# Optimization experiments

Measured on AMD Instinct MI355X. Metric: run time of the kernel, lower is better.

## Reference

```python
import jax, jax.numpy as jnp
import numpy as np

N = 50000
E = 800000
IN_DIM = 128
HID = 128
HEADS = 8
OUT_DIM = 64
LRELU_SLOPE = 0.2


def setup_inputs() -> dict:
    key = jax.random.key(0)
    ks = jax.random.split(key, 10)
    x = jax.random.normal(ks[0], (N, IN_DIM), dtype=jnp.float32)
    edge_index = jax.random.randint(ks[1], (2, E), 0, N, dtype=jnp.int64)
    c1 = HID // HEADS  # 16
    W1 = jax.random.normal(ks[2], (IN_DIM, HID), dtype=jnp.float32) * (1.0 / np.sqrt(IN_DIM))
    as1 = jax.random.normal(ks[3], (HEADS, c1), dtype=jnp.float32) * 0.1
    ad1 = jax.random.normal(ks[4], (HEADS, c1), dtype=jnp.float32) * 0.1
    b1 = jnp.zeros((HID,), dtype=jnp.float32)
    W2 = jax.random.normal(ks[5], (HID, OUT_DIM), dtype=jnp.float32) * (1.0 / np.sqrt(HID))
    as2 = jax.random.normal(ks[6], (1, OUT_DIM), dtype=jnp.float32) * 0.1
    ad2 = jax.random.normal(ks[7], (1, OUT_DIM), dtype=jnp.float32) * 0.1
    b2 = jnp.zeros((OUT_DIM,), dtype=jnp.float32)
    return {"x": x, "edge_index": edge_index, "W1": W1, "as1": as1, "ad1": ad1,
            "b1": b1, "W2": W2, "as2": as2, "ad2": ad2, "b2": b2}


def gat_conv(x, src, dst, W, a_src, a_dst, b, heads, ch, concat):
    n = x.shape[0]
    h = (x @ W).reshape(n, heads, ch)               # [N,H,C]
    alpha_s = jnp.sum(h * a_src, axis=-1)           # [N,H]
    alpha_d = jnp.sum(h * a_dst, axis=-1)           # [N,H]
    e = jax.nn.leaky_relu(alpha_s[src] + alpha_d[dst], LRELU_SLOPE)  # [E,H]
    m = jax.ops.segment_max(e, dst, num_segments=n)  # per-dst max (self-loops guarantee nonempty)
    e = jnp.exp(e - m[dst])
    denom = jax.ops.segment_sum(e, dst, num_segments=n)
    alpha = e / (denom[dst] + 1e-16)                # [E,H]
    msg = h[src] * alpha[:, :, None]                # [E,H,C]
    out = jax.ops.segment_sum(msg, dst, num_segments=n)  # [N,H,C]
    out = out.reshape(n, heads * ch) if concat else out.mean(axis=1)
    return out + b


def reference(x, edge_index, W1, as1, ad1, b1, W2, as2, ad2, b2):
    n = x.shape[0]
    loops = jnp.arange(n, dtype=edge_index.dtype)
    src = jnp.concatenate([edge_index[0], loops])   # PyG GATConv adds self-loops
    dst = jnp.concatenate([edge_index[1], loops])
    # layer 1: GATBlock (dropout is identity at eval), heads=8, concat, ELU
    h = gat_conv(x, src, dst, W1, as1, ad1, b1, HEADS, HID // HEADS, True)
    h = jax.nn.elu(h)
    # final conv: heads=1, concat=False
    out = gat_conv(h, src, dst, W2, as2, ad2, b2, 1, OUT_DIM, False)
    return jax.nn.log_softmax(out, axis=1)
```

## Files before the change

kernel.cpp:

```cpp
#include <hip/hip_runtime.h>
#include <hip/hip_bf16.h>
#include <math.h>

#define IN_DIM 128
#define HID 128
#define HEADS 8
#define OUT_DIM 64
#define SLOPE 0.2f
#define BSHIFT 7
#define BCAP 4096
#define BCAPSHIFT 12
#define EPT 8
#define G1 256
#define G2 256

typedef short bf16x8 __attribute__((ext_vector_type(8)));
typedef float f32x4 __attribute__((ext_vector_type(4)));

__device__ __forceinline__ float lrelu(float x) { return fmaxf(x, SLOPE * x); }
__device__ __forceinline__ float bf2f(unsigned u) { return __uint_as_float(u << 16); }
__device__ __forceinline__ unsigned short f2bf(float f) {
    unsigned u = __float_as_uint(f);
    return (unsigned short)((u + 0x7FFF + ((u >> 16) & 1)) >> 16);
}

__device__ __forceinline__ void bscatter_body(
    int blk, int* smem, const int* __restrict__ idx,
    int* __restrict__ gcursor, unsigned* __restrict__ bucket_buf,
    int E, int N, int NB) {
    int* hist = smem;
    int* base = smem + 512;
    int* s_nz = smem + 1024;
    int t = threadIdx.x;
    for (int i = t; i < NB; i += 256) hist[i] = 0;
    if (t == 0) *s_nz = 0;
    __syncthreads();
    {
        int nz = (idx[2 * t + 1] != 0) + (idx[2 * t + 513] != 0);
        if (nz) atomicAdd(s_nz, nz);
    }
    __syncthreads();
    int flag = (*s_nz > 16) ? 1 : 0;
    int e0 = blk * (256 * EPT);
    int EN = E + N;
    unsigned ent[EPT];
    int bid[EPT];
    int loc[EPT];
#pragma unroll
    for (int k = 0; k < EPT; k++) {
        int e = e0 + k * 256 + t;
        bid[k] = -1;
        if (e < EN) {
            int src, dst;
            if (e < E) {
                if (flag) { src = idx[e]; dst = idx[E + e]; }
                else      { src = idx[2 * e]; dst = idx[2 * (E + e)]; }
            } else {
                src = dst = e - E;
            }
            int b = dst >> BSHIFT;
            bid[k] = b;
            ent[k] = ((unsigned)(dst & ((1 << BSHIFT) - 1)) << 16) | (unsigned)src;
            loc[k] = atomicAdd(&hist[b], 1);
        }
    }
    __syncthreads();
    for (int i = t; i < NB; i += 256) {
        int c = hist[i];
        if (c) base[i] = atomicAdd(&gcursor[i], c);
    }
    __syncthreads();
#pragma unroll
    for (int k = 0; k < EPT; k++) {
        if (bid[k] >= 0) {
            int pos = base[bid[k]] + loc[k];
            if (pos < BCAP) bucket_buf[((size_t)bid[k] << BCAPSHIFT) + pos] = ent[k];
        }
    }
}

__device__ __forceinline__ void gemm1_body(
    int blk, short* Wt, const float* __restrict__ x, const float* __restrict__ W1,
    unsigned short* __restrict__ h1g, int N) {
    int t = threadIdx.x;
    for (int id = t; id < 128 * 32; id += 256) {
        int k = id >> 5;
        int n0 = (id & 31) * 4;
        float4 v = *(const float4*)&W1[k * 128 + n0];
        Wt[(n0 + 0) * 136 + k] = (short)f2bf(v.x);
        Wt[(n0 + 1) * 136 + k] = (short)f2bf(v.y);
        Wt[(n0 + 2) * 136 + k] = (short)f2bf(v.z);
        Wt[(n0 + 3) * 136 + k] = (short)f2bf(v.w);
    }
    __syncthreads();
    int wv = t >> 6, lane = t & 63;
    int m = lane & 15, q = lane >> 4;
    int T = (N + 63) >> 6;
    for (int tile = blk; tile < T; tile += G1) {
        int row = tile * 64 + wv * 16 + m;
        f32x4 acc[8];
#pragma unroll
        for (int j = 0; j < 8; j++) acc[j] = (f32x4){0.f, 0.f, 0.f, 0.f};
#pragma unroll
        for (int k0 = 0; k0 < 128; k0 += 32) {
            bf16x8 a = {0, 0, 0, 0, 0, 0, 0, 0};
            if (row < N) {
                const float* xp = &x[(size_t)row * 128 + k0 + q * 8];
                float4 u0 = *(const float4*)xp;
                float4 u1 = *(const float4*)(xp + 4);
                a[0] = (short)f2bf(u0.x); a[1] = (short)f2bf(u0.y);
                a[2] = (short)f2bf(u0.z); a[3] = (short)f2bf(u0.w);
                a[4] = (short)f2bf(u1.x); a[5] = (short)f2bf(u1.y);
                a[6] = (short)f2bf(u1.z); a[7] = (short)f2bf(u1.w);
            }
#pragma unroll
            for (int j = 0; j < 8; j++) {
                bf16x8 b = *(const bf16x8*)&Wt[(j * 16 + m) * 136 + k0 + q * 8];
                acc[j] = __builtin_amdgcn_mfma_f32_16x16x32_bf16(a, b, acc[j], 0, 0, 0);
            }
        }
        int rbase = tile * 64 + wv * 16 + q * 4;
#pragma unroll
        for (int r = 0; r < 4; r++) {
            int rr = rbase + r;
            if (rr < N) {
#pragma unroll
                for (int j = 0; j < 8; j++)
                    h1g[(size_t)rr * 128 + j * 16 + m] = f2bf(acc[j][r]);
            }
        }
    }
}

__global__ __launch_bounds__(256) void k1_kernel(
    const int* __restrict__ idx, int* __restrict__ gcursor,
    unsigned* __restrict__ bucket_buf,
    const float* __restrict__ x, const float* __restrict__ W1,
    unsigned short* __restrict__ h1g, int E, int N, int NB, int GS) {
    __shared__ long long smem[4352];
    if ((int)blockIdx.x < GS)
        bscatter_body(blockIdx.x, (int*)smem, idx, gcursor, bucket_buf, E, N, NB);
    else
        gemm1_body(blockIdx.x - GS, (short*)smem, x, W1, h1g, N);
}

__device__ __forceinline__ void bsort_body(
    int b, const int* __restrict__ gcursor, const unsigned* __restrict__ bucket_buf,
    int* __restrict__ row_start, int* __restrict__ sorted_src, int N, int NB) {
    __shared__ int cnt[128];
    __shared__ int cur[128];
    __shared__ int red[4];
    __shared__ int s_w0;
    int t = threadIdx.x;
    if (t < 128) cnt[t] = 0;
    int partial = 0;
    for (int i = t; i < b; i += 256) partial += min(gcursor[i], BCAP);
#pragma unroll
    for (int msk = 32; msk > 0; msk >>= 1) partial += __shfl_xor(partial, msk, 64);
    if ((t & 63) == 0) red[t >> 6] = partial;
    __syncthreads();
    int bbase = red[0] + red[1] + red[2] + red[3];
    int c = min(gcursor[b], BCAP);
    const unsigned* buf = bucket_buf + ((size_t)b << BCAPSHIFT);
    for (int i = t; i < c; i += 256)
        atomicAdd(&cnt[(buf[i] >> 16) & 127], 1);
    __syncthreads();
    int v = (t < 128) ? cnt[t] : 0;
    int lane = t & 63;
    int incl = v;
#pragma unroll
    for (int off = 1; off < 64; off <<= 1) {
        int u = __shfl_up(incl, off, 64);
        if (lane >= off) incl += u;
    }
    if (t == 63) s_w0 = incl;
    __syncthreads();
    if (t < 128) {
        int excl = incl - v + ((t >= 64) ? s_w0 : 0);
        int pos = bbase + excl;
        cur[t] = pos;
        int node = (b << BSHIFT) + t;
        if (node <= N) row_start[node] = pos;
    }
    __syncthreads();
    for (int i = t; i < c; i += 256) {
        unsigned e = buf[i];
        int pos = atomicAdd(&cur[(e >> 16) & 127], 1);
        sorted_src[pos] = (int)(e & 0xFFFFu);
    }
}

__device__ __forceinline__ void alpha1_body(
    int blk, const unsigned short* __restrict__ h1g,
    const float* __restrict__ a_s, const float* __restrict__ a_d,
    float* __restrict__ as_n, float* __restrict__ ad_n, int N) {
    int gid = blk * 256 + threadIdx.x;
    if (gid >= N * 8) return;
    int n = gid >> 3, hd = gid & 7;
    const uint4* hp = (const uint4*)(h1g + (size_t)n * 128 + hd * 16);
    uint4 u0 = hp[0], u1 = hp[1];
    unsigned uu[8] = {u0.x, u0.y, u0.z, u0.w, u1.x, u1.y, u1.z, u1.w};
    const float* sp = a_s + hd * 16;
    const float* dp = a_d + hd * 16;
    float s = 0.f, d = 0.f;
#pragma unroll
    for (int k = 0; k < 8; k++) {
        float lo = bf2f(uu[k] & 0xffffu), hi = bf2f(uu[k] >> 16);
        s += lo * sp[2 * k] + hi * sp[2 * k + 1];
        d += lo * dp[2 * k] + hi * dp[2 * k + 1];
    }
    as_n[gid] = s;
    ad_n[gid] = d;
}

__global__ __launch_bounds__(256) void k2_kernel(
    const int* __restrict__ gcursor, const unsigned* __restrict__ bucket_buf,
    int* __restrict__ row_start, int* __restrict__ sorted_src,
    const unsigned short* __restrict__ h1g,
    const float* __restrict__ a_s, const float* __restrict__ a_d,
    float* __restrict__ as_n, float* __restrict__ ad_n, int N, int NB, int EN) {
    if (blockIdx.x == 0 && threadIdx.x < 8) sorted_src[EN + threadIdx.x] = 0;
    if ((int)blockIdx.x < NB)
        bsort_body(blockIdx.x, gcursor, bucket_buf, row_start, sorted_src, N, NB);
    else
        alpha1_body(blockIdx.x - NB, h1g, a_s, a_d, as_n, ad_n, N);
}

__global__ __launch_bounds__(256) void agg1_kernel(
    const int* __restrict__ row_start, const int* __restrict__ sorted_src,
    const float* __restrict__ as_n, const float* __restrict__ ad_n,
    const unsigned short* __restrict__ h1g, const float* __restrict__ b1,
    unsigned short* __restrict__ h1act, int N) {
    int node = blockIdx.x * 4 + (threadIdx.x >> 6);
    int lane = threadIdx.x & 63;
    if (node >= N) return;
    int slot = lane >> 4, cg = lane & 15;
    int e8 = lane >> 3, hd8 = lane & 7;
    int wl_a = (slot << 3) | (cg >> 1);
    int wl_b = ((slot + 4) << 3) | (cg >> 1);
    float ad_w = ad_n[node * 8 + hd8];
    int beg = row_start[node], end = row_start[node + 1];
    float acc[8];
#pragma unroll
    for (int k = 0; k < 8; k++) acc[k] = 0.f;
    float denom = 0.f;
    for (int i = beg; i < end; i += 8) {
        int se = sorted_src[i + e8];
        float w = __expf(lrelu(as_n[se * 8 + hd8] + ad_w));
        w = (i + e8 < end) ? w : 0.f;
        float wva = __shfl(w, wl_a, 64);
        float wvb = __shfl(w, wl_b, 64);
        int sga = __shfl(se, wl_a, 64);
        int sgb = __shfl(se, wl_b, 64);
        uint4 hva = *(const uint4*)&h1g[(size_t)sga * 128 + cg * 8];
        uint4 hvb = *(const uint4*)&h1g[(size_t)sgb * 128 + cg * 8];
        acc[0] += wva * bf2f(hva.x & 0xffffu) + wvb * bf2f(hvb.x & 0xffffu);
        acc[1] += wva * bf2f(hva.x >> 16)     + wvb * bf2f(hvb.x >> 16);
        acc[2] += wva * bf2f(hva.y & 0xffffu) + wvb * bf2f(hvb.y & 0xffffu);
        acc[3] += wva * bf2f(hva.y >> 16)     + wvb * bf2f(hvb.y >> 16);
        acc[4] += wva * bf2f(hva.z & 0xffffu) + wvb * bf2f(hvb.z & 0xffffu);
        acc[5] += wva * bf2f(hva.z >> 16)     + wvb * bf2f(hvb.z >> 16);
        acc[6] += wva * bf2f(hva.w & 0xffffu) + wvb * bf2f(hvb.w & 0xffffu);
        acc[7] += wva * bf2f(hva.w >> 16)     + wvb * bf2f(hvb.w >> 16);
        denom += wva + wvb;
    }
#pragma unroll
    for (int msk = 16; msk < 64; msk <<= 1) {
#pragma unroll
        for (int k = 0; k < 8; k++) acc[k] += __shfl_xor(acc[k], msk, 64);
        denom += __shfl_xor(denom, msk, 64);
    }
    if (slot == 0) {
        float inv = 1.f / (denom + 1e-16f);
        int c0 = cg * 8;
        unsigned ow[4];
#pragma unroll
        for (int p = 0; p < 4; p++) {
            float v0 = acc[2 * p] * inv + b1[c0 + 2 * p];
            float v1 = acc[2 * p + 1] * inv + b1[c0 + 2 * p + 1];
            v0 = (v0 > 0.f) ? v0 : (__expf(v0) - 1.f);
            v1 = (v1 > 0.f) ? v1 : (__expf(v1) - 1.f);
            ow[p] = (unsigned)f2bf(v0) | ((unsigned)f2bf(v1) << 16);
        }
        *(uint4*)&h1act[(size_t)node * 128 + c0] = make_uint4(ow[0], ow[1], ow[2], ow[3]);
    }
}

__global__ __launch_bounds__(256) void gemm2_kernel(
    const unsigned short* __restrict__ h1act, const float* __restrict__ W2,
    const float* __restrict__ a_s, const float* __restrict__ a_d,
    unsigned short* __restrict__ h2g, float* __restrict__ as_n,
    float* __restrict__ ad_n, int N) {
    __shared__ short Wt[64 * 136];
    int t = threadIdx.x;
    for (int id = t; id < 128 * 16; id += 256) {
        int k = id >> 4;
        int n0 = (id & 15) * 4;
        float4 v = *(const float4*)&W2[k * 64 + n0];
        Wt[(n0 + 0) * 136 + k] = (short)f2bf(v.x);
        Wt[(n0 + 1) * 136 + k] = (short)f2bf(v.y);
        Wt[(n0 + 2) * 136 + k] = (short)f2bf(v.z);
        Wt[(n0 + 3) * 136 + k] = (short)f2bf(v.w);
    }
    __syncthreads();
    int wv = t >> 6, lane = t & 63;
    int m = lane & 15, q = lane >> 4;
    float asl[4], adl[4];
#pragma unroll
    for (int j = 0; j < 4; j++) { asl[j] = a_s[j * 16 + m]; adl[j] = a_d[j * 16 + m]; }
    int T = (N + 63) >> 6;
    for (int tile = blockIdx.x; tile < T; tile += G2) {
        int row = tile * 64 + wv * 16 + m;
        f32x4 acc[4];
#pragma unroll
        for (int j = 0; j < 4; j++) acc[j] = (f32x4){0.f, 0.f, 0.f, 0.f};
#pragma unroll
        for (int k0 = 0; k0 < 128; k0 += 32) {
            bf16x8 a = {0, 0, 0, 0, 0, 0, 0, 0};
            if (row < N) a = *(const bf16x8*)&h1act[(size_t)row * 128 + k0 + q * 8];
#pragma unroll
            for (int j = 0; j < 4; j++) {
                bf16x8 b = *(const bf16x8*)&Wt[(j * 16 + m) * 136 + k0 + q * 8];
                acc[j] = __builtin_amdgcn_mfma_f32_16x16x32_bf16(a, b, acc[j], 0, 0, 0);
            }
        }
        int rbase = tile * 64 + wv * 16 + q * 4;
#pragma unroll
        for (int r = 0; r < 4; r++) {
            int rr = rbase + r;
            float s = 0.f, d = 0.f;
#pragma unroll
            for (int j = 0; j < 4; j++) {
                s += acc[j][r] * asl[j];
                d += acc[j][r] * adl[j];
            }
#pragma unroll
            for (int msk = 8; msk > 0; msk >>= 1) {
                s += __shfl_xor(s, msk, 64);
                d += __shfl_xor(d, msk, 64);
            }
            if (rr < N) {
                if (m == 0) { as_n[rr] = s; ad_n[rr] = d; }
#pragma unroll
                for (int j = 0; j < 4; j++)
                    h2g[(size_t)rr * 64 + j * 16 + m] = f2bf(acc[j][r]);
            }
        }
    }
}

__global__ __launch_bounds__(256) void agg2_kernel(
    const int* __restrict__ row_start, const int* __restrict__ sorted_src,
    const float* __restrict__ as_n, const float* __restrict__ ad_n,
    const unsigned short* __restrict__ h2g, const float* __restrict__ b2,
    float* __restrict__ out, int N) {
    int node = blockIdx.x * 4 + (threadIdx.x >> 6);
    int lane = threadIdx.x & 63;
    if (node >= N) return;
    int slot = lane >> 4, cg = lane & 15;
    int e8 = lane & 7;
    float adv = ad_n[node];
    int beg = row_start[node], end = row_start[node + 1];
    float acc[4];
#pragma unroll
    for (int k = 0; k < 4; k++) acc[k] = 0.f;
    float denom = 0.f;
    for (int i = beg; i < end; i += 8) {
        int se = sorted_src[i + e8];
        float w = __expf(lrelu(as_n[se] + adv));
        w = (i + e8 < end) ? w : 0.f;
        float wva = __shfl(w, slot, 64);
        float wvb = __shfl(w, slot + 4, 64);
        int sga = __shfl(se, slot, 64);
        int sgb = __shfl(se, slot + 4, 64);
        uint2 hva = *(const uint2*)&h2g[(size_t)sga * 64 + cg * 4];
        uint2 hvb = *(const uint2*)&h2g[(size_t)sgb * 64 + cg * 4];
        acc[0] += wva * bf2f(hva.x & 0xffffu) + wvb * bf2f(hvb.x & 0xffffu);
        acc[1] += wva * bf2f(hva.x >> 16)     + wvb * bf2f(hvb.x >> 16);
        acc[2] += wva * bf2f(hva.y & 0xffffu) + wvb * bf2f(hvb.y & 0xffffu);
        acc[3] += wva * bf2f(hva.y >> 16)     + wvb * bf2f(hvb.y >> 16);
        denom += wva + wvb;
    }
#pragma unroll
    for (int msk = 16; msk < 64; msk <<= 1) {
#pragma unroll
        for (int k = 0; k < 4; k++) acc[k] += __shfl_xor(acc[k], msk, 64);
        denom += __shfl_xor(denom, msk, 64);
    }
    if (slot == 0) {
        float inv = 1.f / (denom + 1e-16f);
        int c0 = cg * 4;
        float v[4];
#pragma unroll
        for (int k = 0; k < 4; k++) v[k] = acc[k] * inv + b2[c0 + k];
        float m = fmaxf(fmaxf(v[0], v[1]), fmaxf(v[2], v[3]));
#pragma unroll
        for (int msk = 8; msk > 0; msk >>= 1) m = fmaxf(m, __shfl_xor(m, msk, 64));
        float ex = __expf(v[0] - m) + __expf(v[1] - m) + __expf(v[2] - m) + __expf(v[3] - m);
#pragma unroll
        for (int msk = 8; msk > 0; msk >>= 1) ex += __shfl_xor(ex, msk, 64);
        float lse = m + __logf(ex);
        float4 ov = make_float4(v[0] - lse, v[1] - lse, v[2] - lse, v[3] - lse);
        *(float4*)&out[(size_t)node * 64 + c0] = ov;
    }
}

extern "C" void kernel_launch(void* const* d_in, const int* in_sizes, int n_in,
                              void* d_out, int out_size, void* d_ws, size_t ws_size,
                              hipStream_t stream) {
    const float* x   = (const float*)d_in[0];
    const int*   idx = (const int*)d_in[1];
    const float* W1  = (const float*)d_in[2];
    const float* as1 = (const float*)d_in[3];
    const float* ad1 = (const float*)d_in[4];
    const float* b1  = (const float*)d_in[5];
    const float* W2  = (const float*)d_in[6];
    const float* as2 = (const float*)d_in[7];
    const float* ad2 = (const float*)d_in[8];
    const float* b2  = (const float*)d_in[9];
    float* out = (float*)d_out;

    const int N = in_sizes[0] / IN_DIM;
    const int E = in_sizes[1] / 2;
    const int EN = E + N;
    const int NB = (N + (1 << BSHIFT) - 1) >> BSHIFT;
    const int GS = (EN + 256 * EPT - 1) / (256 * EPT);
    const int A1 = (N * 8 + 255) / 256;

    unsigned short* h1g   = (unsigned short*)d_ws;
    unsigned short* h1act = h1g + (size_t)N * 128;
    unsigned short* h2g   = h1act + (size_t)N * 128;
    float* as1n = (float*)(h2g + (size_t)N * 64);
    float* ad1n = as1n + (size_t)N * 8;
    float* as2n = ad1n + (size_t)N * 8;
    float* ad2n = as2n + (size_t)N;
    int* row_start  = (int*)(ad2n + (size_t)N);
    int* gcursor    = row_start + N + 1;
    unsigned* bucket_buf = (unsigned*)(gcursor + 512);
    int* sorted_src = (int*)(bucket_buf + ((size_t)NB << BCAPSHIFT));
    (void)ws_size; (void)n_in; (void)out_size;

    hipMemsetAsync(gcursor, 0, 512 * sizeof(int), stream);

    k1_kernel<<<GS + G1, 256, 0, stream>>>(idx, gcursor, bucket_buf,
                                           x, W1, h1g, E, N, NB, GS);
    k2_kernel<<<NB + A1, 256, 0, stream>>>(gcursor, bucket_buf, row_start, sorted_src,
                                           h1g, as1, ad1, as1n, ad1n, N, NB, EN);
    agg1_kernel<<<(N + 3) / 4, 256, 0, stream>>>(row_start, sorted_src, as1n, ad1n, h1g, b1, h1act, N);
    gemm2_kernel<<<G2, 256, 0, stream>>>(h1act, W2, as2, ad2, h2g, as2n, ad2n, N);
    agg2_kernel<<<(N + 3) / 4, 256, 0, stream>>>(row_start, sorted_src, as2n, ad2n, h2g, b2, out, N);
}
```

Before: 218.6 us.

## Stage bucket scatter and per-bucket sort through LDS for coalesced global writes

In the bucket-scatter phase each block now prefix-sums its local histogram and writes its edges into shared memory in bucket order, then streams them to bucket_buf with consecutive threads. The bucket sort likewise places sorted sources in an LDS array first and copies them out contiguously. Both aim to replace random scattered global stores with mostly coalesced ones. The cost is extra shared memory (about 16 KB more per block in each phase), which can lower occupancy, plus additional barriers and prefix-sum work.

```diff
diff --git a/kernel.cpp b/kernel.cpp
--- a/kernel.cpp
+++ b/kernel.cpp
@@ -28,19 +28,23 @@
     int blk, int* smem, const int* __restrict__ idx,
     int* __restrict__ gcursor, unsigned* __restrict__ bucket_buf,
     int E, int N, int NB) {
-    int* hist = smem;
-    int* base = smem + 512;
-    int* s_nz = smem + 1024;
+    int* hist  = smem;
+    int* gbase = smem + 512;
+    int* lbase = smem + 1024;
+    int* wtot  = smem + 1536;
+    int* misc  = smem + 1540;
+    unsigned* sent = (unsigned*)(smem + 1552);
+    unsigned* spos = (unsigned*)(smem + 3600);
     int t = threadIdx.x;
-    for (int i = t; i < NB; i += 256) hist[i] = 0;
-    if (t == 0) *s_nz = 0;
+    for (int i = t; i < 512; i += 256) hist[i] = 0;
+    if (t == 0) misc[1] = 0;
     __syncthreads();
     {
         int nz = (idx[2 * t + 1] != 0) + (idx[2 * t + 513] != 0);
-        if (nz) atomicAdd(s_nz, nz);
-    }
-    __syncthreads();
-    int flag = (*s_nz > 16) ? 1 : 0;
+        if (nz) atomicAdd(&misc[1], nz);
+    }
+    __syncthreads();
+    int flag = (misc[1] > 16) ? 1 : 0;
     int e0 = blk * (256 * EPT);
     int EN = E + N;
     unsigned ent[EPT];
@@ -65,17 +69,44 @@
         }
     }
     __syncthreads();
-    for (int i = t; i < NB; i += 256) {
+    int i0 = 2 * t;
+    int a = hist[i0], b2 = hist[i0 + 1];
+    int ps = a + b2;
+    int lane = t & 63, w = t >> 6;
+    int incl = ps;
+#pragma unroll
+    for (int off = 1; off < 64; off <<= 1) {
+        int u = __shfl_up(incl, off, 64);
+        if (lane >= off) incl += u;
+    }
+    if (lane == 63) wtot[w] = incl;
+    __syncthreads();
+    int woff = 0;
+    for (int k = 0; k < w; k++) woff += wtot[k];
+    int ex0 = woff + incl - ps;
+    lbase[i0] = ex0;
+    lbase[i0 + 1] = ex0 + a;
+    if (t == 255) misc[0] = woff + incl;
+    for (int i = t; i < 512; i += 256) {
         int c = hist[i];
-        if (c) base[i] = atomicAdd(&gcursor[i], c);
+        gbase[i] = c ? atomicAdd(&gcursor[i], c) : 0;
     }
     __syncthreads();
 #pragma unroll
     for (int k = 0; k < EPT; k++) {
         if (bid[k] >= 0) {
-            int pos = base[bid[k]] + loc[k];
-            if (pos < BCAP) bucket_buf[((size_t)bid[k] << BCAPSHIFT) + pos] = ent[k];
-        }
+            int p = lbase[bid[k]] + loc[k];
+            int pib = gbase[bid[k]] + loc[k];
+            sent[p] = ent[k];
+            spos[p] = (pib < BCAP) ? (((unsigned)bid[k] << BCAPSHIFT) | (unsigned)pib)
+                                   : 0xFFFFFFFFu;
+        }
+    }
+    __syncthreads();
+    int tot = misc[0];
+    for (int i = t; i < tot; i += 256) {
+        unsigned sp = spos[i];
+        if (sp != 0xFFFFFFFFu) bucket_buf[sp] = sent[i];
     }
 }
 
@@ -151,6 +182,7 @@
     __shared__ int cur[128];
     __shared__ int red[4];
     __shared__ int s_w0;
+    __shared__ int srt[BCAP];
     int t = threadIdx.x;
     if (t < 128) cnt[t] = 0;
     int partial = 0;
@@ -177,17 +209,19 @@
     __syncthreads();
     if (t < 128) {
         int excl = incl - v + ((t >= 64) ? s_w0 : 0);
-        int pos = bbase + excl;
-        cur[t] = pos;
+        cur[t] = excl;
         int node = (b << BSHIFT) + t;
-        if (node <= N) row_start[node] = pos;
+        if (node <= N) row_start[node] = bbase + excl;
     }
     __syncthreads();
     for (int i = t; i < c; i += 256) {
         unsigned e = buf[i];
-        int pos = atomicAdd(&cur[(e >> 16) & 127], 1);
-        sorted_src[pos] = (int)(e & 0xFFFFu);
-    }
+        int lp = atomicAdd(&cur[(e >> 16) & 127], 1);
+        srt[lp] = (int)(e & 0xFFFFu);
+    }
+    __syncthreads();
+    for (int i = t; i < c; i += 256)
+        sorted_src[bbase + i] = srt[i];
 }
 
 __device__ __forceinline__ void alpha1_body(
```

After: 215.8 us. No clear change (-1.3%).
